# Kernel tuning notes

Hardware: AMD Instinct MI355X
Metric: run time of the kernel (lower is better)

## Reference

```python
import jax, jax.numpy as jnp
import numpy as np

EPSILON = 1.0
SIGMA = 1.0
R_CUT = 2.5 * SIGMA  # module stores r_cut * sigma
BOX = 20.0  # box side length for uniform particle positions


def setup_inputs() -> dict:
    key = jax.random.key(0)
    N = 8192
    positions = jax.random.uniform(key, (N, 3), dtype=jnp.float32) * BOX
    return {"positions": positions}


def reference(positions) -> jnp.ndarray:
    # positions: [N, 3]
    N = positions.shape[0]
    diff = positions[:, None, :] - positions[None, :, :]      # [N, N, 3]
    r2 = jnp.sum(diff * diff, axis=-1)                        # [N, N]
    r = jnp.sqrt(r2)
    # upper triangle (i < j) and strict cutoff r_ij < r_cut, as in forward()
    iu = jnp.arange(N)
    pair_mask = (iu[:, None] < iu[None, :]) & (r < R_CUT)
    # avoid div-by-zero on the (masked) diagonal
    safe_r2 = jnp.where(pair_mask, r2, jnp.float32(1.0))
    sr2 = (SIGMA * SIGMA) / safe_r2
    sr6 = sr2 * sr2 * sr2
    sr12 = sr6 * sr6
    e_pair = 4.0 * EPSILON * (sr12 - sr6)                     # [N, N]
    energy = jnp.sum(jnp.where(pair_mask, e_pair, jnp.float32(0.0)))
    return energy
```

## Files before the change

kernel.cpp:

```cpp
#include <hip/hip_runtime.h>

#define RC2    6.25f
#define CINV   0.4f
#define NC     8
#define NCELLS 512
#define MAXOWN 128
#define MAXNB  512
#define POISON 0xAAAAAAAAu
#define NT     512

__device__ __forceinline__ float wave_reduce_sum(float v) {
    #pragma unroll
    for (int off = 32; off > 0; off >>= 1)
        v += __shfl_down(v, off, 64);
    return v;
}

__global__ __launch_bounds__(NT, 2) void lj_fused(const float4* __restrict__ p4, int N,
                                                  float* __restrict__ partial,
                                                  unsigned int* __restrict__ ticket,
                                                  float* __restrict__ out) {
    const int c  = blockIdx.x;
    const int cx = c & 7, cy = (c >> 3) & 7, cz = c >> 6;
    const int tid = threadIdx.x;

    __shared__ float4 own[MAXOWN];
    __shared__ float4 nbl[MAXNB];
    __shared__ int s_nOwn, s_nNb;
    if (tid == 0) { s_nOwn = 0; s_nNb = 0; }
    __syncthreads();

    const int nChunk = N >> 2;
    #pragma unroll 4
    for (int q = tid; q < nChunk; q += NT) {
        float4 A = p4[3 * q + 0];
        float4 B = p4[3 * q + 1];
        float4 C = p4[3 * q + 2];
        float px[4] = {A.x, A.w, B.z, C.y};
        float py[4] = {A.y, B.x, B.w, C.z};
        float pz[4] = {A.z, B.y, C.x, C.w};
        #pragma unroll
        for (int u = 0; u < 4; ++u) {
            int dx = min((int)(px[u] * CINV), NC - 1) - cx + 1;
            int dy = min((int)(py[u] * CINV), NC - 1) - cy + 1;
            int dz = min((int)(pz[u] * CINV), NC - 1) - cz + 1;
            if (((unsigned)dx < 3u) & ((unsigned)dy < 3u) & ((unsigned)dz < 3u)) {
                int code = (dz * 3 + dy) * 3 + dx;
                if (code == 13) {
                    int s = atomicAdd(&s_nOwn, 1);
                    if (s < MAXOWN) own[s] = make_float4(px[u], py[u], pz[u], 0.0f);
                } else if (code > 13) {
                    int s = atomicAdd(&s_nNb, 1);
                    if (s < MAXNB) nbl[s] = make_float4(px[u], py[u], pz[u], 0.0f);
                }
            }
        }
    }
    __syncthreads();

    const int nOwn = min(s_nOwn, MAXOWN);
    const int nNb  = min(s_nNb, MAXNB);

    float e = 0.0f;
    for (int i = 0; i < nOwn; ++i) {
        float4 pi = own[i];
        for (int j = i + 1 + tid; j < nOwn; j += NT) {
            float4 pj = own[j];
            float ddx = pi.x - pj.x;
            float ddy = pi.y - pj.y;
            float ddz = pi.z - pj.z;
            float r2 = ddx * ddx + ddy * ddy + ddz * ddz;
            bool ok = (r2 < RC2);
            float inv = ok ? __builtin_amdgcn_rcpf(r2) : 0.0f;
            float sr6 = inv * inv * inv;
            e += sr6 * sr6 - sr6;
        }
        for (int j = tid; j < nNb; j += NT) {
            float4 pj = nbl[j];
            float ddx = pi.x - pj.x;
            float ddy = pi.y - pj.y;
            float ddz = pi.z - pj.z;
            float r2 = ddx * ddx + ddy * ddy + ddz * ddz;
            bool ok = (r2 < RC2);
            float inv = ok ? __builtin_amdgcn_rcpf(r2) : 0.0f;
            float sr6 = inv * inv * inv;
            e += sr6 * sr6 - sr6;
        }
    }

    __shared__ float ssum[NT / 64];
    float w = wave_reduce_sum(e);
    if ((tid & 63) == 0) ssum[tid >> 6] = w;
    __syncthreads();

    __shared__ int s_last;
    if (tid == 0) {
        float bsum = 0.0f;
        #pragma unroll
        for (int q = 0; q < NT / 64; ++q) bsum += ssum[q];
        float oldp = atomicExch(&partial[c], bsum);
        unsigned int dep = __float_as_uint(oldp) & 0u;
        asm volatile("" : "+v"(dep));
        unsigned int old = atomicAdd(ticket, 1u + dep);
        s_last = (old == NCELLS - 1u) || (old == POISON + (NCELLS - 1u));
    }
    __syncthreads();

    if (s_last) {
        float v = 0.0f;
        for (int idx = tid; idx < NCELLS; idx += NT)
            v += atomicAdd(&partial[idx], 0.0f);
        float w2 = wave_reduce_sum(v);
        __shared__ float s2[NT / 64];
        if ((tid & 63) == 0) s2[tid >> 6] = w2;
        __syncthreads();
        if (tid == 0) {
            float tot = 0.0f;
            #pragma unroll
            for (int q = 0; q < NT / 64; ++q) tot += s2[q];
            out[0] = 4.0f * tot;
            __hip_atomic_store(ticket, 0u, __ATOMIC_RELAXED, __HIP_MEMORY_SCOPE_AGENT);
        }
    }
}

extern "C" void kernel_launch(void* const* d_in, const int* in_sizes, int n_in,
                              void* d_out, int out_size, void* d_ws, size_t ws_size,
                              hipStream_t stream) {
    const float4* p4 = (const float4*)d_in[0];
    float* out = (float*)d_out;

    unsigned int* ticket  = (unsigned int*)d_ws;
    float*        partial = (float*)((char*)d_ws + 64);

    int N = in_sizes[0] / 3;

    lj_fused<<<NCELLS, NT, 0, stream>>>(p4, N, partial, ticket, out);
}
```

Baseline: 18.98 us.

## Process two adjacent cells per block to halve full-array position scans

Each block now owns two x-adjacent cells instead of one, halving the grid to 256 blocks. Every block still scans all positions to bin particles, so this halves the total redundant global scan work. Each half of the block (256 threads) computes the pair energy for one cell. The cost is fewer blocks on a GPU with many CUs, less parallelism in the compute phase, and twice the shared memory per block.

After: 20.07 us. +5.7%, slower.

```diff
diff --git a/kernel.cpp b/kernel.cpp
--- a/kernel.cpp
+++ b/kernel.cpp
@@ -3,7 +3,7 @@
 #define RC2    6.25f
 #define CINV   0.4f
 #define NC     8
-#define NCELLS 512
+#define NBLK   256
 #define MAXOWN 128
 #define MAXNB  512
 #define POISON 0xAAAAAAAAu
@@ -20,14 +20,16 @@
                                                   float* __restrict__ partial,
                                                   unsigned int* __restrict__ ticket,
                                                   float* __restrict__ out) {
-    const int c  = blockIdx.x;
-    const int cx = c & 7, cy = (c >> 3) & 7, cz = c >> 6;
+    const int b   = blockIdx.x;
+    const int cx0 = (b & 3) * 2;
+    const int cy  = (b >> 2) & 7;
+    const int cz  = b >> 5;
     const int tid = threadIdx.x;
 
-    __shared__ float4 own[MAXOWN];
-    __shared__ float4 nbl[MAXNB];
-    __shared__ int s_nOwn, s_nNb;
-    if (tid == 0) { s_nOwn = 0; s_nNb = 0; }
+    __shared__ float4 own[2][MAXOWN];
+    __shared__ float4 nbl[2][MAXNB];
+    __shared__ int s_nOwn[2], s_nNb[2];
+    if (tid < 2) { s_nOwn[tid] = 0; s_nNb[tid] = 0; }
     __syncthreads();
 
     const int nChunk = N >> 2;
@@ -41,31 +43,47 @@
         float pz[4] = {A.z, B.y, C.x, C.w};
         #pragma unroll
         for (int u = 0; u < 4; ++u) {
-            int dx = min((int)(px[u] * CINV), NC - 1) - cx + 1;
-            int dy = min((int)(py[u] * CINV), NC - 1) - cy + 1;
-            int dz = min((int)(pz[u] * CINV), NC - 1) - cz + 1;
-            if (((unsigned)dx < 3u) & ((unsigned)dy < 3u) & ((unsigned)dz < 3u)) {
-                int code = (dz * 3 + dy) * 3 + dx;
-                if (code == 13) {
-                    int s = atomicAdd(&s_nOwn, 1);
-                    if (s < MAXOWN) own[s] = make_float4(px[u], py[u], pz[u], 0.0f);
-                } else if (code > 13) {
-                    int s = atomicAdd(&s_nNb, 1);
-                    if (s < MAXNB) nbl[s] = make_float4(px[u], py[u], pz[u], 0.0f);
+            int dx0 = min((int)(px[u] * CINV), NC - 1) - cx0 + 1;
+            int dy  = min((int)(py[u] * CINV), NC - 1) - cy + 1;
+            int dz  = min((int)(pz[u] * CINV), NC - 1) - cz + 1;
+            if (((unsigned)dy < 3u) & ((unsigned)dz < 3u)) {
+                int rowc = (dz * 3 + dy) * 3;
+                if ((unsigned)dx0 < 3u) {
+                    int code = rowc + dx0;
+                    if (code == 13) {
+                        int s = atomicAdd(&s_nOwn[0], 1);
+                        if (s < MAXOWN) own[0][s] = make_float4(px[u], py[u], pz[u], 0.0f);
+                    } else if (code > 13) {
+                        int s = atomicAdd(&s_nNb[0], 1);
+                        if (s < MAXNB) nbl[0][s] = make_float4(px[u], py[u], pz[u], 0.0f);
+                    }
+                }
+                int dx1 = dx0 - 1;
+                if ((unsigned)dx1 < 3u) {
+                    int code = rowc + dx1;
+                    if (code == 13) {
+                        int s = atomicAdd(&s_nOwn[1], 1);
+                        if (s < MAXOWN) own[1][s] = make_float4(px[u], py[u], pz[u], 0.0f);
+                    } else if (code > 13) {
+                        int s = atomicAdd(&s_nNb[1], 1);
+                        if (s < MAXNB) nbl[1][s] = make_float4(px[u], py[u], pz[u], 0.0f);
+                    }
                 }
             }
         }
     }
     __syncthreads();
 
-    const int nOwn = min(s_nOwn, MAXOWN);
-    const int nNb  = min(s_nNb, MAXNB);
+    const int sel  = tid >> 8;
+    const int ltid = tid & 255;
+    const int nOwnS = min(s_nOwn[sel], MAXOWN);
+    const int nNbS  = min(s_nNb[sel], MAXNB);
 
     float e = 0.0f;
-    for (int i = 0; i < nOwn; ++i) {
-        float4 pi = own[i];
-        for (int j = i + 1 + tid; j < nOwn; j += NT) {
-            float4 pj = own[j];
+    for (int i = 0; i < nOwnS; ++i) {
+        float4 pi = own[sel][i];
+        for (int j = i + 1 + ltid; j < nOwnS; j += 256) {
+            float4 pj = own[sel][j];
             float ddx = pi.x - pj.x;
             float ddy = pi.y - pj.y;
             float ddz = pi.z - pj.z;
@@ -75,8 +93,8 @@
             float sr6 = inv * inv * inv;
             e += sr6 * sr6 - sr6;
         }
-        for (int j = tid; j < nNb; j += NT) {
-            float4 pj = nbl[j];
+        for (int j = ltid; j < nNbS; j += 256) {
+            float4 pj = nbl[sel][j];
             float ddx = pi.x - pj.x;
             float ddy = pi.y - pj.y;
             float ddz = pi.z - pj.z;
@@ -98,17 +116,17 @@
         float bsum = 0.0f;
         #pragma unroll
         for (int q = 0; q < NT / 64; ++q) bsum += ssum[q];
-        float oldp = atomicExch(&partial[c], bsum);
+        float oldp = atomicExch(&partial[b], bsum);
         unsigned int dep = __float_as_uint(oldp) & 0u;
         asm volatile("" : "+v"(dep));
         unsigned int old = atomicAdd(ticket, 1u + dep);
-        s_last = (old == NCELLS - 1u) || (old == POISON + (NCELLS - 1u));
+        s_last = (old == NBLK - 1u) || (old == POISON + (NBLK - 1u));
     }
     __syncthreads();
 
     if (s_last) {
         float v = 0.0f;
-        for (int idx = tid; idx < NCELLS; idx += NT)
+        for (int idx = tid; idx < NBLK; idx += NT)
             v += atomicAdd(&partial[idx], 0.0f);
         float w2 = wave_reduce_sum(v);
         __shared__ float s2[NT / 64];
@@ -135,5 +153,5 @@
 
     int N = in_sizes[0] / 3;
 
-    lj_fused<<<NCELLS, NT, 0, stream>>>(p4, N, partial, ticket, out);
+    lj_fused<<<NBLK, NT, 0, stream>>>(p4, N, partial, ticket, out);
 }
```
